# Performance work log

Measured on AMD Instinct MI355X. Metric: run time of the kernel, lower is better.

## Reference

```python
import jax, jax.numpy as jnp
import numpy as np

B, D, C, P = 64, 262144, 4, 4096  # batch, original_dim, c, proj_dim


def setup_inputs() -> dict:
    key = jax.random.key(0)
    kx, ki, ks = jax.random.split(key, 3)
    x = jax.random.normal(kx, (B, D), dtype=jnp.float32)
    rand_indices = jax.random.randint(ki, (D, C), 0, P, dtype=jnp.int64)
    rand_sign_bits = jax.random.randint(ks, (D, C), 0, 2, dtype=jnp.int32)
    return {"x": x, "rand_indices": rand_indices, "rand_sign_bits": rand_sign_bits}


def reference(x, rand_indices, rand_sign_bits):
    # signs in {-1, +1}, matching (randint(0,2)*2 - 1) in the torch module
    signs = (2 * rand_sign_bits - 1).astype(x.dtype)          # [D, C]
    idx = rand_indices.reshape(-1)                             # [D*C]
    vals = (x[:, :, None] * signs[None, :, :]).reshape(x.shape[0], -1)  # [B, D*C]
    # scatter-add each signed value into its hashed projection slot
    project = lambda v: jax.ops.segment_sum(v, idx, num_segments=P)
    return jax.vmap(project)(vals)                             # [B, P]
```

## Files before the change

### kernel.cpp

```cpp
#include <hip/hip_runtime.h>
#include <hip/hip_bf16.h>
#include <hip/hip_fp16.h>


constexpr int B_DIM = 64;
constexpr int D_DIM = 262144;
constexpr int P_DIM = 4096;

constexpr int NDS   = 64;
constexpr int SLICE = D_DIM / NDS;
constexpr int NBIN  = 16;
constexpr int NSC   = 16;
constexpr int SC_D  = SLICE / NSC;
constexpr int BCAP  = 128;
constexpr int NHB   = 32;
constexpr int WPB   = 8;
constexpr int PR_W  = 16;
constexpr int NPR   = P_DIM / PR_W;
constexpr int LCAP  = 128;

constexpr size_t REG_OFF   = 0;
constexpr size_t REG_BYTES = (size_t)NDS * NSC * NBIN * BCAP * 4;
constexpr size_t CNT_OFF   = REG_OFF + REG_BYTES;
constexpr size_t CNT_BYTES = (size_t)NDS * NSC * NBIN * 4;
constexpr size_t XT_OFF    = CNT_OFF + CNT_BYTES;
constexpr size_t XT_BYTES  = (size_t)D_DIM * B_DIM * 2;
constexpr size_t PART_OFF  = XT_OFF + XT_BYTES;
constexpr size_t PART_BYTES = (size_t)NPR * NDS * PR_W * B_DIM * 2;
constexpr size_t WS_NEED   = PART_OFF + PART_BYTES;

__global__ __launch_bounds__(512) void k_binpack(
    const int* __restrict__ idx, const int* __restrict__ sgn,
    unsigned* __restrict__ reg, int* __restrict__ cnt) {
    const int w = threadIdx.x >> 6, lane = threadIdx.x & 63;
    const int dslice = blockIdx.x >> 1;
    const int half   = blockIdx.x & 1;
    const int sc     = half * 8 + w;
    const int d0     = dslice * SLICE + sc * SC_D;
    unsigned* regw = reg + ((size_t)(dslice * NSC + sc) * NBIN) * BCAP;
    const unsigned long long lmask = (1ull << lane) - 1ull;

    unsigned cb[16];
    #pragma unroll
    for (int b = 0; b < 16; ++b) cb[b] = 0;

    #pragma unroll
    for (int step = 0; step < SC_D / 64; ++step) {
        const int dli = step * 64 + lane;
        const int4 iv = reinterpret_cast<const int4*>(idx)[d0 + dli];
        const int4 sv = reinterpret_cast<const int4*>(sgn)[d0 + dli];
        const unsigned rowbyte = (unsigned)((sc * SC_D + dli) << 7);
        #pragma unroll
        for (int c = 0; c < 4; ++c) {
            const unsigned p = ((unsigned)((c==0)?iv.x:(c==1)?iv.y:(c==2)?iv.z:iv.w)) & 4095u;
            const unsigned s = ((unsigned)((c==0)?sv.x:(c==1)?sv.y:(c==2)?sv.z:sv.w)) & 1u;
            const unsigned e = rowbyte | ((p & 255u) << 19) | ((s ^ 1u) << 31);
            const unsigned bin = p >> 8;
            unsigned pos = 0;
            #pragma unroll
            for (int b = 0; b < 16; ++b) {
                const unsigned long long m = __ballot(bin == (unsigned)b);
                if (bin == (unsigned)b) pos = cb[b] + (unsigned)__popcll(m & lmask);
                cb[b] += (unsigned)__popcll(m);
            }
            if (pos < (unsigned)BCAP) regw[bin * BCAP + pos] = e;
        }
    }
    unsigned cval = 0;
    #pragma unroll
    for (int b = 0; b < 16; ++b) {
        const unsigned cc = cb[b] < (unsigned)BCAP ? cb[b] : (unsigned)BCAP;
        cval = (lane == b) ? cc : cval;
    }
    if (lane < 16) cnt[(dslice * NSC + sc) * NBIN + lane] = (int)cval;
}

__device__ __forceinline__ unsigned short f32_to_bf16_rne(float f) {
    unsigned u = __float_as_uint(f);
    u += 0x7FFFu + ((u >> 16) & 1u);
    return (unsigned short)(u >> 16);
}

__global__ __launch_bounds__(256) void k_transpose(
    const float* __restrict__ x, unsigned short* __restrict__ xTb) {
    __shared__ float tile[64 * 65];
    const int d0 = blockIdx.x * 64;
    const int t = threadIdx.x;
    const int lane = t & 63;
    #pragma unroll
    for (int k = 0; k < 16; ++k) {
        const int b = k * 4 + (t >> 6);
        tile[lane * 65 + b] = x[(size_t)b * D_DIM + d0 + lane];
    }
    __syncthreads();
    #pragma unroll
    for (int k = 0; k < 16; ++k) {
        const int dr = k * 4 + (t >> 6);
        xTb[(size_t)(d0 + dr) * B_DIM + lane] = f32_to_bf16_rne(tile[dr * 65 + lane]);
    }
}

__global__ __launch_bounds__(512, 8) void k_process(
    const unsigned* __restrict__ reg, const int* __restrict__ cnt,
    const unsigned short* __restrict__ xTb, __half* __restrict__ part) {
    __shared__ __half2 hist[WPB][2 * PR_W * 32];
    __shared__ unsigned lst[WPB][LCAP];
    __shared__ int cnts[WPB][WPB];
    __shared__ int baseL[WPB][WPB];
    __shared__ int totals[WPB];

    const int w = threadIdx.x >> 6, lane = threadIdx.x & 63;
    const int dslice = blockIdx.x & 63;
    const int hb  = blockIdx.x >> 6;
    const int bin = hb >> 1, half = hb & 1;

    __half2* hw = hist[w];
    {
        unsigned* h32 = reinterpret_cast<unsigned*>(hw);
        #pragma unroll
        for (int k = 0; k < 16; ++k) h32[k * 64 + lane] = 0u;
    }

    const unsigned long long lmask = (1ull << lane) - 1ull;

    unsigned er[4];
    int n0 = 0, n1 = 0;
    int c0 = 0, c1 = 0, c2 = 0, c3 = 0, c4 = 0, c5 = 0, c6 = 0, c7 = 0;
    #pragma unroll
    for (int sc2 = 0; sc2 < 2; ++sc2) {
        const int sc = 2 * w + sc2;
        const int n  = cnt[(dslice * NSC + sc) * NBIN + bin];
        const unsigned* list = reg + ((size_t)((dslice * NSC + sc) * NBIN + bin)) * BCAP;
        if (sc2 == 0) n0 = n; else n1 = n;
        #pragma unroll
        for (int b = 0; b < 2; ++b) {
            const int i = b * 64 + lane;
            const unsigned e = (i < n) ? list[i] : 0u;
            er[sc2 * 2 + b] = e;
            const unsigned po8 = (e >> 19) & 255u;
            const bool valid = (i < n) && ((int)(po8 >> 7) == half);
            const unsigned t = valid ? ((po8 >> 4) & 7u) : 0xFFu;
            const unsigned long long m0 = __ballot(t == 0u);
            const unsigned long long m1 = __ballot(t == 1u);
            const unsigned long long m2 = __ballot(t == 2u);
            const unsigned long long m3 = __ballot(t == 3u);
            const unsigned long long m4 = __ballot(t == 4u);
            const unsigned long long m5 = __ballot(t == 5u);
            const unsigned long long m6 = __ballot(t == 6u);
            const unsigned long long m7 = __ballot(t == 7u);
            c0 += __popcll(m0); c1 += __popcll(m1);
            c2 += __popcll(m2); c3 += __popcll(m3);
            c4 += __popcll(m4); c5 += __popcll(m5);
            c6 += __popcll(m6); c7 += __popcll(m7);
        }
    }
    {
        int cval = 0;
        cval = (lane == 0) ? c0 : cval; cval = (lane == 1) ? c1 : cval;
        cval = (lane == 2) ? c2 : cval; cval = (lane == 3) ? c3 : cval;
        cval = (lane == 4) ? c4 : cval; cval = (lane == 5) ? c5 : cval;
        cval = (lane == 6) ? c6 : cval; cval = (lane == 7) ? c7 : cval;
        if (lane < 8) cnts[w][lane] = cval;
    }
    __syncthreads();

    if (w == 0 && lane < 8) {
        int run = 0;
        #pragma unroll
        for (int ww = 0; ww < 8; ++ww) { baseL[lane][ww] = run; run += cnts[ww][lane]; }
        totals[lane] = run;
    }
    __syncthreads();

    c0 = c1 = c2 = c3 = c4 = c5 = c6 = c7 = 0;
    #pragma unroll
    for (int sc2 = 0; sc2 < 2; ++sc2) {
        const int n = (sc2 == 0) ? n0 : n1;
        #pragma unroll
        for (int b = 0; b < 2; ++b) {
            const int i = b * 64 + lane;
            const unsigned e = er[sc2 * 2 + b];
            const unsigned po8 = (e >> 19) & 255u;
            const bool valid = (i < n) && ((int)(po8 >> 7) == half);
            const unsigned t = valid ? ((po8 >> 4) & 7u) : 0xFFu;
            const unsigned long long m0 = __ballot(t == 0u);
            const unsigned long long m1 = __ballot(t == 1u);
            const unsigned long long m2 = __ballot(t == 2u);
            const unsigned long long m3 = __ballot(t == 3u);
            const unsigned long long m4 = __ballot(t == 4u);
            const unsigned long long m5 = __ballot(t == 5u);
            const unsigned long long m6 = __ballot(t == 6u);
            const unsigned long long m7 = __ballot(t == 7u);
            if (valid) {
                const unsigned long long mt =
                    t < 4u ? (t < 2u ? (t == 0u ? m0 : m1) : (t == 2u ? m2 : m3))
                           : (t < 6u ? (t == 4u ? m4 : m5) : (t == 6u ? m6 : m7));
                const int cbase =
                    t < 4u ? (t < 2u ? (t == 0u ? c0 : c1) : (t == 2u ? c2 : c3))
                           : (t < 6u ? (t == 4u ? c4 : c5) : (t == 6u ? c6 : c7));
                const int pos = baseL[t][w] + cbase + (int)__popcll(mt & lmask);
                if (pos < LCAP) lst[t][pos] = e;
            }
            c0 += __popcll(m0); c1 += __popcll(m1);
            c2 += __popcll(m2); c3 += __popcll(m3);
            c4 += __popcll(m4); c5 += __popcll(m5);
            c6 += __popcll(m6); c7 += __popcll(m7);
        }
    }
    __syncthreads();

    const char* xs_c = reinterpret_cast<const char*>(xTb) + (size_t)dslice * SLICE * 128;
    const unsigned li4 = (unsigned)(lane & 31) * 4u;
    const bool hi = lane >= 32;
    const unsigned l31 = (unsigned)(lane & 31);
    const int n = totals[w] < LCAP ? totals[w] : LCAP;
    const unsigned* L = lst[w];

    int i = 0;
    for (; i + 8 <= n; i += 8) {
        const uint4 A  = *reinterpret_cast<const uint4*>(L + i);
        const uint4 Bv = *reinterpret_cast<const uint4*>(L + i + 4);
        const unsigned e0 = __builtin_amdgcn_readfirstlane(A.x);
        const unsigned e1 = __builtin_amdgcn_readfirstlane(A.y);
        const unsigned e2 = __builtin_amdgcn_readfirstlane(A.z);
        const unsigned e3 = __builtin_amdgcn_readfirstlane(A.w);
        const unsigned e4 = __builtin_amdgcn_readfirstlane(Bv.x);
        const unsigned e5 = __builtin_amdgcn_readfirstlane(Bv.y);
        const unsigned e6 = __builtin_amdgcn_readfirstlane(Bv.z);
        const unsigned e7 = __builtin_amdgcn_readfirstlane(Bv.w);
        const unsigned va0 = (hi ? (e4 & 0x7FFFFu) : (e0 & 0x7FFFFu)) + li4;
        const unsigned va1 = (hi ? (e5 & 0x7FFFFu) : (e1 & 0x7FFFFu)) + li4;
        const unsigned va2 = (hi ? (e6 & 0x7FFFFu) : (e2 & 0x7FFFFu)) + li4;
        const unsigned va3 = (hi ? (e7 & 0x7FFFFu) : (e3 & 0x7FFFFu)) + li4;
        const unsigned d0 = *reinterpret_cast<const unsigned*>(xs_c + va0);
        const unsigned d1 = *reinterpret_cast<const unsigned*>(xs_c + va1);
        const unsigned d2 = *reinterpret_cast<const unsigned*>(xs_c + va2);
        const unsigned d3 = *reinterpret_cast<const unsigned*>(xs_c + va3);

        const unsigned pL0 = (e0 >> 19) & 15u, pL1 = (e1 >> 19) & 15u;
        const unsigned pL2 = (e2 >> 19) & 15u, pL3 = (e3 >> 19) & 15u;
        const unsigned pH0 = (e4 >> 19) & 15u, pH1 = (e5 >> 19) & 15u;
        const unsigned pH2 = (e6 >> 19) & 15u, pH3 = (e7 >> 19) & 15u;

        __half2 v[4];
        #pragma unroll
        for (int k = 0; k < 4; ++k) {
            const unsigned dv = (k == 0) ? d0 : (k == 1) ? d1 : (k == 2) ? d2 : d3;
            const unsigned eL = (k == 0) ? e0 : (k == 1) ? e1 : (k == 2) ? e2 : e3;
            const unsigned eH = (k == 0) ? e4 : (k == 1) ? e5 : (k == 2) ? e6 : e7;
            const float flo = __uint_as_float(dv << 16);
            const float fhh = __uint_as_float(dv & 0xFFFF0000u);
            unsigned pkb = __builtin_bit_cast(unsigned, __floats2half2_rn(flo, fhh));
            const unsigned sm = hi ? (eH & 0x80000000u) : (eL & 0x80000000u);
            pkb ^= sm ? 0x80008000u : 0u;
            v[k] = __builtin_bit_cast(__half2, pkb);
        }

        const __half2 zero2 = __builtin_bit_cast(__half2, 0u);
        {
            const bool m01 = hi ? (pH0 == pH1) : (pL0 == pL1);
            v[1] = m01 ? __hadd2(v[1], v[0]) : v[1];  v[0] = m01 ? zero2 : v[0];
            const bool m02 = hi ? (pH0 == pH2) : (pL0 == pL2);
            v[2] = m02 ? __hadd2(v[2], v[0]) : v[2];  v[0] = m02 ? zero2 : v[0];
            const bool m12 = hi ? (pH1 == pH2) : (pL1 == pL2);
            v[2] = m12 ? __hadd2(v[2], v[1]) : v[2];  v[1] = m12 ? zero2 : v[1];
            const bool m03 = hi ? (pH0 == pH3) : (pL0 == pL3);
            v[3] = m03 ? __hadd2(v[3], v[0]) : v[3];  v[0] = m03 ? zero2 : v[0];
            const bool m13 = hi ? (pH1 == pH3) : (pL1 == pL3);
            v[3] = m13 ? __hadd2(v[3], v[1]) : v[3];  v[1] = m13 ? zero2 : v[1];
            const bool m23 = hi ? (pH2 == pH3) : (pL2 == pL3);
            v[3] = m23 ? __hadd2(v[3], v[2]) : v[3];  v[2] = m23 ? zero2 : v[2];
        }

        const unsigned a0 = (hi ? (512u + pH0 * 32u) : (pL0 * 32u)) + l31;
        const unsigned a1 = (hi ? (512u + pH1 * 32u) : (pL1 * 32u)) + l31;
        const unsigned a2 = (hi ? (512u + pH2 * 32u) : (pL2 * 32u)) + l31;
        const unsigned a3 = (hi ? (512u + pH3 * 32u) : (pL3 * 32u)) + l31;
        const __half2 h0 = hw[a0];
        const __half2 h1 = hw[a1];
        const __half2 h2v = hw[a2];
        const __half2 h3 = hw[a3];
        hw[a0] = __hadd2(h0, v[0]);
        hw[a1] = __hadd2(h1, v[1]);
        hw[a2] = __hadd2(h2v, v[2]);
        hw[a3] = __hadd2(h3, v[3]);
    }
    for (; i + 2 <= n; i += 2) {
        const unsigned eA = __builtin_amdgcn_readfirstlane(L[i]);
        const unsigned eB = __builtin_amdgcn_readfirstlane(L[i + 1]);
        const unsigned va = (hi ? (eB & 0x7FFFFu) : (eA & 0x7FFFFu)) + li4;
        const unsigned dv = *reinterpret_cast<const unsigned*>(xs_c + va);
        const float flo = __uint_as_float(dv << 16);
        const float fhh = __uint_as_float(dv & 0xFFFF0000u);
        unsigned pkb = __builtin_bit_cast(unsigned, __floats2half2_rn(flo, fhh));
        const unsigned sm = hi ? (eB & 0x80000000u) : (eA & 0x80000000u);
        pkb ^= sm ? 0x80008000u : 0u;
        const unsigned po = hi ? ((eB >> 19) & 15u) : ((eA >> 19) & 15u);
        const unsigned a = (hi ? (512u + po * 32u) : (po * 32u)) + l31;
        hw[a] = __hadd2(hw[a], __builtin_bit_cast(__half2, pkb));
    }
    if (i < n) {
        const unsigned eA = __builtin_amdgcn_readfirstlane(L[i]);
        if (!hi) {
            const unsigned va = (eA & 0x7FFFFu) + li4;
            const unsigned dv = *reinterpret_cast<const unsigned*>(xs_c + va);
            const float flo = __uint_as_float(dv << 16);
            const float fhh = __uint_as_float(dv & 0xFFFF0000u);
            unsigned pkb = __builtin_bit_cast(unsigned, __floats2half2_rn(flo, fhh));
            pkb ^= (eA & 0x80000000u) ? 0x80008000u : 0u;
            const unsigned a = ((eA >> 19) & 15u) * 32u + l31;
            hw[a] = __hadd2(hw[a], __builtin_bit_cast(__half2, pkb));
        }
    }

    unsigned* wp32 = reinterpret_cast<unsigned*>(
        part + ((size_t)((hb * WPB + w) * NDS + dslice)) * (PR_W * B_DIM));
    #pragma unroll
    for (int k = 0; k < 8; ++k) {
        const int idxw = k * 64 + lane;
        const __half2 s = __hadd2(hw[idxw], hw[512 + idxw]);
        wp32[idxw] = __builtin_bit_cast(unsigned, s);
    }
}

__global__ __launch_bounds__(256) void k_reduce(
    const __half* __restrict__ part, float* __restrict__ out) {
    const int pr = blockIdx.x;
    const int t  = threadIdx.x;

    float4 acc = make_float4(0.f, 0.f, 0.f, 0.f);
    const size_t base = (size_t)pr * NDS * (PR_W * B_DIM);
    for (int ds = 0; ds < NDS; ++ds) {
        const uint2 pv = *reinterpret_cast<const uint2*>(
            part + base + (size_t)ds * (PR_W * B_DIM) + t * 4);
        const __half2 h0 = __builtin_bit_cast(__half2, pv.x);
        const __half2 h1 = __builtin_bit_cast(__half2, pv.y);
        acc.x += __half2float(h0.x); acc.y += __half2float(h0.y);
        acc.z += __half2float(h1.x); acc.w += __half2float(h1.y);
    }

    __shared__ float st[16][65];
    const int po = (t * 4) >> 6;
    const int b0 = (t * 4) & 63;
    st[po][b0]     = acc.x; st[po][b0 + 1] = acc.y;
    st[po][b0 + 2] = acc.z; st[po][b0 + 3] = acc.w;
    __syncthreads();

    #pragma unroll
    for (int k = 0; k < 4; ++k) {
        const int flat = k * 256 + t;
        const int b = flat >> 4, poo = flat & 15;
        out[(size_t)b * P_DIM + pr * PR_W + poo] = st[poo][b];
    }
}

__device__ __forceinline__ float signed_val(float x, int s) {
    return __uint_as_float(__float_as_uint(x) ^ (((unsigned)(s ^ 1)) << 31));
}

__global__ __launch_bounds__(1024) void sjlt_hist_fb(
    const float* __restrict__ x, const int* __restrict__ idx,
    const int* __restrict__ sgn, float* __restrict__ out) {
    __shared__ float hist[2][P_DIM];
    for (int i = threadIdx.x; i < 2 * P_DIM; i += 1024) (&hist[0][0])[i] = 0.0f;
    __syncthreads();
    const int chunk = blockIdx.x, bg = blockIdx.y;
    const int d0 = chunk * (D_DIM / 16), b0 = bg * 2;
    const float* xr0 = x + (size_t)b0 * D_DIM + d0;
    const float* xr1 = xr0 + D_DIM;
    const int4* iv4 = reinterpret_cast<const int4*>(idx) + d0;
    const int4* sv4 = reinterpret_cast<const int4*>(sgn) + d0;
    for (int t = threadIdx.x; t < D_DIM / 16; t += 1024) {
        const int4 iv = iv4[t]; const int4 sv = sv4[t];
        const float x0 = xr0[t], x1 = xr1[t];
        unsafeAtomicAdd(&hist[0][iv.x], signed_val(x0, sv.x));
        unsafeAtomicAdd(&hist[0][iv.y], signed_val(x0, sv.y));
        unsafeAtomicAdd(&hist[0][iv.z], signed_val(x0, sv.z));
        unsafeAtomicAdd(&hist[0][iv.w], signed_val(x0, sv.w));
        unsafeAtomicAdd(&hist[1][iv.x], signed_val(x1, sv.x));
        unsafeAtomicAdd(&hist[1][iv.y], signed_val(x1, sv.y));
        unsafeAtomicAdd(&hist[1][iv.z], signed_val(x1, sv.z));
        unsafeAtomicAdd(&hist[1][iv.w], signed_val(x1, sv.w));
    }
    __syncthreads();
    float* o = out + (size_t)b0 * P_DIM;
    for (int p = threadIdx.x; p < P_DIM; p += 1024) {
        unsafeAtomicAdd(&o[p],         hist[0][p]);
        unsafeAtomicAdd(&o[P_DIM + p], hist[1][p]);
    }
}

extern "C" void kernel_launch(void* const* d_in, const int* in_sizes, int n_in,
                              void* d_out, int out_size, void* d_ws, size_t ws_size,
                              hipStream_t stream) {
    const float* x   = (const float*)d_in[0];
    const int*   idx = (const int*)d_in[1];
    const int*   sgn = (const int*)d_in[2];
    float* out = (float*)d_out;

    if (ws_size >= WS_NEED) {
        char* ws = (char*)d_ws;
        unsigned* reg = (unsigned*)(ws + REG_OFF);
        int* cnt      = (int*)(ws + CNT_OFF);
        unsigned short* xTb = (unsigned short*)(ws + XT_OFF);
        __half* part  = (__half*)(ws + PART_OFF);

        k_binpack<<<NDS * 2, 512, 0, stream>>>(idx, sgn, reg, cnt);
        k_transpose<<<D_DIM / 64, 256, 0, stream>>>(x, xTb);
        k_process<<<NHB * NDS, 512, 0, stream>>>(reg, cnt, xTb, part);
        k_reduce<<<NPR, 256, 0, stream>>>(part, out);
    } else {
        hipMemsetAsync(d_out, 0, (size_t)out_size * sizeof(float), stream);
        dim3 grid(16, 32);
        sjlt_hist_fb<<<grid, 1024, 0, stream>>>(x, idx, sgn, out);
    }
}
```

Before: 77.11 us.

## Group d-slices per process block, store x as fp16, split binpack finer

Each k_process block now loops over four d-slices and accumulates into its shared-memory histogram before writing partials. This cuts the partial buffer and the k_reduce work by a factor of four, at the cost of fewer, longer blocks and extra barriers inside the loop. The transpose now stores x as fp16 rather than bf16, so the per-element bf16-to-fp16 conversion in the inner loop becomes a plain sign XOR. This changes rounding and fp16 range behaviour. k_binpack is relaunched as 256-thread blocks with four blocks per slice, giving more and smaller blocks.

```diff
diff --git a/kernel.cpp b/kernel.cpp
--- a/kernel.cpp
+++ b/kernel.cpp
@@ -14,6 +14,8 @@
 constexpr int SC_D  = SLICE / NSC;
 constexpr int BCAP  = 128;
 constexpr int NHB   = 32;
+constexpr int G_DS  = 4;
+constexpr int NDG   = NDS / G_DS;
 constexpr int WPB   = 8;
 constexpr int PR_W  = 16;
 constexpr int NPR   = P_DIM / PR_W;
@@ -26,17 +28,17 @@
 constexpr size_t XT_OFF    = CNT_OFF + CNT_BYTES;
 constexpr size_t XT_BYTES  = (size_t)D_DIM * B_DIM * 2;
 constexpr size_t PART_OFF  = XT_OFF + XT_BYTES;
-constexpr size_t PART_BYTES = (size_t)NPR * NDS * PR_W * B_DIM * 2;
+constexpr size_t PART_BYTES = (size_t)NPR * NDG * PR_W * B_DIM * 2;
 constexpr size_t WS_NEED   = PART_OFF + PART_BYTES;
 
-__global__ __launch_bounds__(512) void k_binpack(
+__global__ __launch_bounds__(256) void k_binpack(
     const int* __restrict__ idx, const int* __restrict__ sgn,
     unsigned* __restrict__ reg, int* __restrict__ cnt) {
     const int w = threadIdx.x >> 6, lane = threadIdx.x & 63;
-    const int dslice = blockIdx.x >> 1;
-    const int half   = blockIdx.x & 1;
-    const int sc     = half * 8 + w;
-    const int d0     = dslice * SLICE + sc * SC_D;
+    const int dslice  = blockIdx.x >> 2;
+    const int quarter = blockIdx.x & 3;
+    const int sc      = quarter * 4 + w;
+    const int d0      = dslice * SLICE + sc * SC_D;
     unsigned* regw = reg + ((size_t)(dslice * NSC + sc) * NBIN) * BCAP;
     const unsigned long long lmask = (1ull << lane) - 1ull;
 
@@ -75,14 +77,8 @@
     if (lane < 16) cnt[(dslice * NSC + sc) * NBIN + lane] = (int)cval;
 }
 
-__device__ __forceinline__ unsigned short f32_to_bf16_rne(float f) {
-    unsigned u = __float_as_uint(f);
-    u += 0x7FFFu + ((u >> 16) & 1u);
-    return (unsigned short)(u >> 16);
-}
-
 __global__ __launch_bounds__(256) void k_transpose(
-    const float* __restrict__ x, unsigned short* __restrict__ xTb) {
+    const float* __restrict__ x, unsigned short* __restrict__ xTh) {
     __shared__ float tile[64 * 65];
     const int d0 = blockIdx.x * 64;
     const int t = threadIdx.x;
@@ -96,13 +92,14 @@
     #pragma unroll
     for (int k = 0; k < 16; ++k) {
         const int dr = k * 4 + (t >> 6);
-        xTb[(size_t)(d0 + dr) * B_DIM + lane] = f32_to_bf16_rne(tile[dr * 65 + lane]);
+        const __half h = __float2half_rn(tile[dr * 65 + lane]);
+        xTh[(size_t)(d0 + dr) * B_DIM + lane] = __builtin_bit_cast(unsigned short, h);
     }
 }
 
 __global__ __launch_bounds__(512, 8) void k_process(
     const unsigned* __restrict__ reg, const int* __restrict__ cnt,
-    const unsigned short* __restrict__ xTb, __half* __restrict__ part) {
+    const unsigned short* __restrict__ xTh, __half* __restrict__ part) {
     __shared__ __half2 hist[WPB][2 * PR_W * 32];
     __shared__ unsigned lst[WPB][LCAP];
     __shared__ int cnts[WPB][WPB];
@@ -110,8 +107,8 @@
     __shared__ int totals[WPB];
 
     const int w = threadIdx.x >> 6, lane = threadIdx.x & 63;
-    const int dslice = blockIdx.x & 63;
-    const int hb  = blockIdx.x >> 6;
+    const int dg  = blockIdx.x & 15;
+    const int hb  = blockIdx.x >> 4;
     const int bin = hb >> 1, half = hb & 1;
 
     __half2* hw = hist[w];
@@ -122,199 +119,187 @@
     }
 
     const unsigned long long lmask = (1ull << lane) - 1ull;
-
-    unsigned er[4];
-    int n0 = 0, n1 = 0;
-    int c0 = 0, c1 = 0, c2 = 0, c3 = 0, c4 = 0, c5 = 0, c6 = 0, c7 = 0;
-    #pragma unroll
-    for (int sc2 = 0; sc2 < 2; ++sc2) {
-        const int sc = 2 * w + sc2;
-        const int n  = cnt[(dslice * NSC + sc) * NBIN + bin];
-        const unsigned* list = reg + ((size_t)((dslice * NSC + sc) * NBIN + bin)) * BCAP;
-        if (sc2 == 0) n0 = n; else n1 = n;
-        #pragma unroll
-        for (int b = 0; b < 2; ++b) {
-            const int i = b * 64 + lane;
-            const unsigned e = (i < n) ? list[i] : 0u;
-            er[sc2 * 2 + b] = e;
-            const unsigned po8 = (e >> 19) & 255u;
-            const bool valid = (i < n) && ((int)(po8 >> 7) == half);
-            const unsigned t = valid ? ((po8 >> 4) & 7u) : 0xFFu;
-            const unsigned long long m0 = __ballot(t == 0u);
-            const unsigned long long m1 = __ballot(t == 1u);
-            const unsigned long long m2 = __ballot(t == 2u);
-            const unsigned long long m3 = __ballot(t == 3u);
-            const unsigned long long m4 = __ballot(t == 4u);
-            const unsigned long long m5 = __ballot(t == 5u);
-            const unsigned long long m6 = __ballot(t == 6u);
-            const unsigned long long m7 = __ballot(t == 7u);
-            c0 += __popcll(m0); c1 += __popcll(m1);
-            c2 += __popcll(m2); c3 += __popcll(m3);
-            c4 += __popcll(m4); c5 += __popcll(m5);
-            c6 += __popcll(m6); c7 += __popcll(m7);
-        }
-    }
-    {
-        int cval = 0;
-        cval = (lane == 0) ? c0 : cval; cval = (lane == 1) ? c1 : cval;
-        cval = (lane == 2) ? c2 : cval; cval = (lane == 3) ? c3 : cval;
-        cval = (lane == 4) ? c4 : cval; cval = (lane == 5) ? c5 : cval;
-        cval = (lane == 6) ? c6 : cval; cval = (lane == 7) ? c7 : cval;
-        if (lane < 8) cnts[w][lane] = cval;
-    }
-    __syncthreads();
-
-    if (w == 0 && lane < 8) {
-        int run = 0;
-        #pragma unroll
-        for (int ww = 0; ww < 8; ++ww) { baseL[lane][ww] = run; run += cnts[ww][lane]; }
-        totals[lane] = run;
-    }
-    __syncthreads();
-
-    c0 = c1 = c2 = c3 = c4 = c5 = c6 = c7 = 0;
-    #pragma unroll
-    for (int sc2 = 0; sc2 < 2; ++sc2) {
-        const int n = (sc2 == 0) ? n0 : n1;
-        #pragma unroll
-        for (int b = 0; b < 2; ++b) {
-            const int i = b * 64 + lane;
-            const unsigned e = er[sc2 * 2 + b];
-            const unsigned po8 = (e >> 19) & 255u;
-            const bool valid = (i < n) && ((int)(po8 >> 7) == half);
-            const unsigned t = valid ? ((po8 >> 4) & 7u) : 0xFFu;
-            const unsigned long long m0 = __ballot(t == 0u);
-            const unsigned long long m1 = __ballot(t == 1u);
-            const unsigned long long m2 = __ballot(t == 2u);
-            const unsigned long long m3 = __ballot(t == 3u);
-            const unsigned long long m4 = __ballot(t == 4u);
-            const unsigned long long m5 = __ballot(t == 5u);
-            const unsigned long long m6 = __ballot(t == 6u);
-            const unsigned long long m7 = __ballot(t == 7u);
-            if (valid) {
-                const unsigned long long mt =
-                    t < 4u ? (t < 2u ? (t == 0u ? m0 : m1) : (t == 2u ? m2 : m3))
-                           : (t < 6u ? (t == 4u ? m4 : m5) : (t == 6u ? m6 : m7));
-                const int cbase =
-                    t < 4u ? (t < 2u ? (t == 0u ? c0 : c1) : (t == 2u ? c2 : c3))
-                           : (t < 6u ? (t == 4u ? c4 : c5) : (t == 6u ? c6 : c7));
-                const int pos = baseL[t][w] + cbase + (int)__popcll(mt & lmask);
-                if (pos < LCAP) lst[t][pos] = e;
-            }
-            c0 += __popcll(m0); c1 += __popcll(m1);
-            c2 += __popcll(m2); c3 += __popcll(m3);
-            c4 += __popcll(m4); c5 += __popcll(m5);
-            c6 += __popcll(m6); c7 += __popcll(m7);
-        }
-    }
-    __syncthreads();
-
-    const char* xs_c = reinterpret_cast<const char*>(xTb) + (size_t)dslice * SLICE * 128;
     const unsigned li4 = (unsigned)(lane & 31) * 4u;
     const bool hi = lane >= 32;
     const unsigned l31 = (unsigned)(lane & 31);
-    const int n = totals[w] < LCAP ? totals[w] : LCAP;
-    const unsigned* L = lst[w];
-
-    int i = 0;
-    for (; i + 8 <= n; i += 8) {
-        const uint4 A  = *reinterpret_cast<const uint4*>(L + i);
-        const uint4 Bv = *reinterpret_cast<const uint4*>(L + i + 4);
-        const unsigned e0 = __builtin_amdgcn_readfirstlane(A.x);
-        const unsigned e1 = __builtin_amdgcn_readfirstlane(A.y);
-        const unsigned e2 = __builtin_amdgcn_readfirstlane(A.z);
-        const unsigned e3 = __builtin_amdgcn_readfirstlane(A.w);
-        const unsigned e4 = __builtin_amdgcn_readfirstlane(Bv.x);
-        const unsigned e5 = __builtin_amdgcn_readfirstlane(Bv.y);
-        const unsigned e6 = __builtin_amdgcn_readfirstlane(Bv.z);
-        const unsigned e7 = __builtin_amdgcn_readfirstlane(Bv.w);
-        const unsigned va0 = (hi ? (e4 & 0x7FFFFu) : (e0 & 0x7FFFFu)) + li4;
-        const unsigned va1 = (hi ? (e5 & 0x7FFFFu) : (e1 & 0x7FFFFu)) + li4;
-        const unsigned va2 = (hi ? (e6 & 0x7FFFFu) : (e2 & 0x7FFFFu)) + li4;
-        const unsigned va3 = (hi ? (e7 & 0x7FFFFu) : (e3 & 0x7FFFFu)) + li4;
-        const unsigned d0 = *reinterpret_cast<const unsigned*>(xs_c + va0);
-        const unsigned d1 = *reinterpret_cast<const unsigned*>(xs_c + va1);
-        const unsigned d2 = *reinterpret_cast<const unsigned*>(xs_c + va2);
-        const unsigned d3 = *reinterpret_cast<const unsigned*>(xs_c + va3);
-
-        const unsigned pL0 = (e0 >> 19) & 15u, pL1 = (e1 >> 19) & 15u;
-        const unsigned pL2 = (e2 >> 19) & 15u, pL3 = (e3 >> 19) & 15u;
-        const unsigned pH0 = (e4 >> 19) & 15u, pH1 = (e5 >> 19) & 15u;
-        const unsigned pH2 = (e6 >> 19) & 15u, pH3 = (e7 >> 19) & 15u;
-
-        __half2 v[4];
+
+    for (int ds = 0; ds < G_DS; ++ds) {
+        const int dslice = dg * G_DS + ds;
+
+        unsigned er[4];
+        int n0 = 0, n1 = 0;
+        int c0 = 0, c1 = 0, c2 = 0, c3 = 0, c4 = 0, c5 = 0, c6 = 0, c7 = 0;
         #pragma unroll
-        for (int k = 0; k < 4; ++k) {
-            const unsigned dv = (k == 0) ? d0 : (k == 1) ? d1 : (k == 2) ? d2 : d3;
-            const unsigned eL = (k == 0) ? e0 : (k == 1) ? e1 : (k == 2) ? e2 : e3;
-            const unsigned eH = (k == 0) ? e4 : (k == 1) ? e5 : (k == 2) ? e6 : e7;
-            const float flo = __uint_as_float(dv << 16);
-            const float fhh = __uint_as_float(dv & 0xFFFF0000u);
-            unsigned pkb = __builtin_bit_cast(unsigned, __floats2half2_rn(flo, fhh));
-            const unsigned sm = hi ? (eH & 0x80000000u) : (eL & 0x80000000u);
-            pkb ^= sm ? 0x80008000u : 0u;
-            v[k] = __builtin_bit_cast(__half2, pkb);
-        }
-
-        const __half2 zero2 = __builtin_bit_cast(__half2, 0u);
+        for (int sc2 = 0; sc2 < 2; ++sc2) {
+            const int sc = 2 * w + sc2;
+            const int n  = cnt[(dslice * NSC + sc) * NBIN + bin];
+            const unsigned* list = reg + ((size_t)((dslice * NSC + sc) * NBIN + bin)) * BCAP;
+            if (sc2 == 0) n0 = n; else n1 = n;
+            #pragma unroll
+            for (int b = 0; b < 2; ++b) {
+                const int i = b * 64 + lane;
+                const unsigned e = (i < n) ? list[i] : 0u;
+                er[sc2 * 2 + b] = e;
+                const unsigned po8 = (e >> 19) & 255u;
+                const bool valid = (i < n) && ((int)(po8 >> 7) == half);
+                const unsigned t = valid ? ((po8 >> 4) & 7u) : 0xFFu;
+                c0 += __popcll(__ballot(t == 0u)); c1 += __popcll(__ballot(t == 1u));
+                c2 += __popcll(__ballot(t == 2u)); c3 += __popcll(__ballot(t == 3u));
+                c4 += __popcll(__ballot(t == 4u)); c5 += __popcll(__ballot(t == 5u));
+                c6 += __popcll(__ballot(t == 6u)); c7 += __popcll(__ballot(t == 7u));
+            }
+        }
         {
-            const bool m01 = hi ? (pH0 == pH1) : (pL0 == pL1);
-            v[1] = m01 ? __hadd2(v[1], v[0]) : v[1];  v[0] = m01 ? zero2 : v[0];
-            const bool m02 = hi ? (pH0 == pH2) : (pL0 == pL2);
-            v[2] = m02 ? __hadd2(v[2], v[0]) : v[2];  v[0] = m02 ? zero2 : v[0];
-            const bool m12 = hi ? (pH1 == pH2) : (pL1 == pL2);
-            v[2] = m12 ? __hadd2(v[2], v[1]) : v[2];  v[1] = m12 ? zero2 : v[1];
-            const bool m03 = hi ? (pH0 == pH3) : (pL0 == pL3);
-            v[3] = m03 ? __hadd2(v[3], v[0]) : v[3];  v[0] = m03 ? zero2 : v[0];
-            const bool m13 = hi ? (pH1 == pH3) : (pL1 == pL3);
-            v[3] = m13 ? __hadd2(v[3], v[1]) : v[3];  v[1] = m13 ? zero2 : v[1];
-            const bool m23 = hi ? (pH2 == pH3) : (pL2 == pL3);
-            v[3] = m23 ? __hadd2(v[3], v[2]) : v[3];  v[2] = m23 ? zero2 : v[2];
-        }
-
-        const unsigned a0 = (hi ? (512u + pH0 * 32u) : (pL0 * 32u)) + l31;
-        const unsigned a1 = (hi ? (512u + pH1 * 32u) : (pL1 * 32u)) + l31;
-        const unsigned a2 = (hi ? (512u + pH2 * 32u) : (pL2 * 32u)) + l31;
-        const unsigned a3 = (hi ? (512u + pH3 * 32u) : (pL3 * 32u)) + l31;
-        const __half2 h0 = hw[a0];
-        const __half2 h1 = hw[a1];
-        const __half2 h2v = hw[a2];
-        const __half2 h3 = hw[a3];
-        hw[a0] = __hadd2(h0, v[0]);
-        hw[a1] = __hadd2(h1, v[1]);
-        hw[a2] = __hadd2(h2v, v[2]);
-        hw[a3] = __hadd2(h3, v[3]);
-    }
-    for (; i + 2 <= n; i += 2) {
-        const unsigned eA = __builtin_amdgcn_readfirstlane(L[i]);
-        const unsigned eB = __builtin_amdgcn_readfirstlane(L[i + 1]);
-        const unsigned va = (hi ? (eB & 0x7FFFFu) : (eA & 0x7FFFFu)) + li4;
-        const unsigned dv = *reinterpret_cast<const unsigned*>(xs_c + va);
-        const float flo = __uint_as_float(dv << 16);
-        const float fhh = __uint_as_float(dv & 0xFFFF0000u);
-        unsigned pkb = __builtin_bit_cast(unsigned, __floats2half2_rn(flo, fhh));
-        const unsigned sm = hi ? (eB & 0x80000000u) : (eA & 0x80000000u);
-        pkb ^= sm ? 0x80008000u : 0u;
-        const unsigned po = hi ? ((eB >> 19) & 15u) : ((eA >> 19) & 15u);
-        const unsigned a = (hi ? (512u + po * 32u) : (po * 32u)) + l31;
-        hw[a] = __hadd2(hw[a], __builtin_bit_cast(__half2, pkb));
-    }
-    if (i < n) {
-        const unsigned eA = __builtin_amdgcn_readfirstlane(L[i]);
-        if (!hi) {
-            const unsigned va = (eA & 0x7FFFFu) + li4;
+            int cval = 0;
+            cval = (lane == 0) ? c0 : cval; cval = (lane == 1) ? c1 : cval;
+            cval = (lane == 2) ? c2 : cval; cval = (lane == 3) ? c3 : cval;
+            cval = (lane == 4) ? c4 : cval; cval = (lane == 5) ? c5 : cval;
+            cval = (lane == 6) ? c6 : cval; cval = (lane == 7) ? c7 : cval;
+            if (lane < 8) cnts[w][lane] = cval;
+        }
+        __syncthreads();
+
+        if (w == 0 && lane < 8) {
+            int run = 0;
+            #pragma unroll
+            for (int ww = 0; ww < 8; ++ww) { baseL[lane][ww] = run; run += cnts[ww][lane]; }
+            totals[lane] = run;
+        }
+        __syncthreads();
+
+        c0 = c1 = c2 = c3 = c4 = c5 = c6 = c7 = 0;
+        #pragma unroll
+        for (int sc2 = 0; sc2 < 2; ++sc2) {
+            const int n = (sc2 == 0) ? n0 : n1;
+            #pragma unroll
+            for (int b = 0; b < 2; ++b) {
+                const int i = b * 64 + lane;
+                const unsigned e = er[sc2 * 2 + b];
+                const unsigned po8 = (e >> 19) & 255u;
+                const bool valid = (i < n) && ((int)(po8 >> 7) == half);
+                const unsigned t = valid ? ((po8 >> 4) & 7u) : 0xFFu;
+                const unsigned long long m0 = __ballot(t == 0u);
+                const unsigned long long m1 = __ballot(t == 1u);
+                const unsigned long long m2 = __ballot(t == 2u);
+                const unsigned long long m3 = __ballot(t == 3u);
+                const unsigned long long m4 = __ballot(t == 4u);
+                const unsigned long long m5 = __ballot(t == 5u);
+                const unsigned long long m6 = __ballot(t == 6u);
+                const unsigned long long m7 = __ballot(t == 7u);
+                if (valid) {
+                    const unsigned long long mt =
+                        t < 4u ? (t < 2u ? (t == 0u ? m0 : m1) : (t == 2u ? m2 : m3))
+                               : (t < 6u ? (t == 4u ? m4 : m5) : (t == 6u ? m6 : m7));
+                    const int cbase =
+                        t < 4u ? (t < 2u ? (t == 0u ? c0 : c1) : (t == 2u ? c2 : c3))
+                               : (t < 6u ? (t == 4u ? c4 : c5) : (t == 6u ? c6 : c7));
+                    const int pos = baseL[t][w] + cbase + (int)__popcll(mt & lmask);
+                    if (pos < LCAP) lst[t][pos] = e;
+                }
+                c0 += __popcll(m0); c1 += __popcll(m1);
+                c2 += __popcll(m2); c3 += __popcll(m3);
+                c4 += __popcll(m4); c5 += __popcll(m5);
+                c6 += __popcll(m6); c7 += __popcll(m7);
+            }
+        }
+        __syncthreads();
+
+        const char* xs_c = reinterpret_cast<const char*>(xTh) + (size_t)dslice * SLICE * 128;
+        const int n = totals[w] < LCAP ? totals[w] : LCAP;
+        const unsigned* L = lst[w];
+
+        int i = 0;
+        for (; i + 8 <= n; i += 8) {
+            const uint4 A  = *reinterpret_cast<const uint4*>(L + i);
+            const uint4 Bv = *reinterpret_cast<const uint4*>(L + i + 4);
+            const unsigned e0 = __builtin_amdgcn_readfirstlane(A.x);
+            const unsigned e1 = __builtin_amdgcn_readfirstlane(A.y);
+            const unsigned e2 = __builtin_amdgcn_readfirstlane(A.z);
+            const unsigned e3 = __builtin_amdgcn_readfirstlane(A.w);
+            const unsigned e4 = __builtin_amdgcn_readfirstlane(Bv.x);
+            const unsigned e5 = __builtin_amdgcn_readfirstlane(Bv.y);
+            const unsigned e6 = __builtin_amdgcn_readfirstlane(Bv.z);
+            const unsigned e7 = __builtin_amdgcn_readfirstlane(Bv.w);
+            const unsigned va0 = (hi ? (e4 & 0x7FFFFu) : (e0 & 0x7FFFFu)) + li4;
+            const unsigned va1 = (hi ? (e5 & 0x7FFFFu) : (e1 & 0x7FFFFu)) + li4;
+            const unsigned va2 = (hi ? (e6 & 0x7FFFFu) : (e2 & 0x7FFFFu)) + li4;
+            const unsigned va3 = (hi ? (e7 & 0x7FFFFu) : (e3 & 0x7FFFFu)) + li4;
+            const unsigned d0 = *reinterpret_cast<const unsigned*>(xs_c + va0);
+            const unsigned d1 = *reinterpret_cast<const unsigned*>(xs_c + va1);
+            const unsigned d2 = *reinterpret_cast<const unsigned*>(xs_c + va2);
+            const unsigned d3 = *reinterpret_cast<const unsigned*>(xs_c + va3);
+
+            const unsigned pL0 = (e0 >> 19) & 15u, pL1 = (e1 >> 19) & 15u;
+            const unsigned pL2 = (e2 >> 19) & 15u, pL3 = (e3 >> 19) & 15u;
+            const unsigned pH0 = (e4 >> 19) & 15u, pH1 = (e5 >> 19) & 15u;
+            const unsigned pH2 = (e6 >> 19) & 15u, pH3 = (e7 >> 19) & 15u;
+
+            __half2 v[4];
+            #pragma unroll
+            for (int k = 0; k < 4; ++k) {
+                const unsigned dv = (k == 0) ? d0 : (k == 1) ? d1 : (k == 2) ? d2 : d3;
+                const unsigned eL = (k == 0) ? e0 : (k == 1) ? e1 : (k == 2) ? e2 : e3;
+                const unsigned eH = (k == 0) ? e4 : (k == 1) ? e5 : (k == 2) ? e6 : e7;
+                const unsigned sm = hi ? (eH & 0x80000000u) : (eL & 0x80000000u);
+                v[k] = __builtin_bit_cast(__half2, dv ^ (sm ? 0x80008000u : 0u));
+            }
+
+            const __half2 zero2 = __builtin_bit_cast(__half2, 0u);
+            {
+                const bool m01 = hi ? (pH0 == pH1) : (pL0 == pL1);
+                v[1] = m01 ? __hadd2(v[1], v[0]) : v[1];  v[0] = m01 ? zero2 : v[0];
+                const bool m02 = hi ? (pH0 == pH2) : (pL0 == pL2);
+                v[2] = m02 ? __hadd2(v[2], v[0]) : v[2];  v[0] = m02 ? zero2 : v[0];
+                const bool m12 = hi ? (pH1 == pH2) : (pL1 == pL2);
+                v[2] = m12 ? __hadd2(v[2], v[1]) : v[2];  v[1] = m12 ? zero2 : v[1];
+                const bool m03 = hi ? (pH0 == pH3) : (pL0 == pL3);
+                v[3] = m03 ? __hadd2(v[3], v[0]) : v[3];  v[0] = m03 ? zero2 : v[0];
+                const bool m13 = hi ? (pH1 == pH3) : (pL1 == pL3);
+                v[3] = m13 ? __hadd2(v[3], v[1]) : v[3];  v[1] = m13 ? zero2 : v[1];
+                const bool m23 = hi ? (pH2 == pH3) : (pL2 == pL3);
+                v[3] = m23 ? __hadd2(v[3], v[2]) : v[3];  v[2] = m23 ? zero2 : v[2];
+            }
+
+            const unsigned a0 = (hi ? (512u + pH0 * 32u) : (pL0 * 32u)) + l31;
+            const unsigned a1 = (hi ? (512u + pH1 * 32u) : (pL1 * 32u)) + l31;
+            const unsigned a2 = (hi ? (512u + pH2 * 32u) : (pL2 * 32u)) + l31;
+            const unsigned a3 = (hi ? (512u + pH3 * 32u) : (pL3 * 32u)) + l31;
+            const __half2 h0 = hw[a0];
+            const __half2 h1 = hw[a1];
+            const __half2 h2v = hw[a2];
+            const __half2 h3 = hw[a3];
+            hw[a0] = __hadd2(h0, v[0]);
+            hw[a1] = __hadd2(h1, v[1]);
+            hw[a2] = __hadd2(h2v, v[2]);
+            hw[a3] = __hadd2(h3, v[3]);
+        }
+        for (; i + 2 <= n; i += 2) {
+            const unsigned eA = __builtin_amdgcn_readfirstlane(L[i]);
+            const unsigned eB = __builtin_amdgcn_readfirstlane(L[i + 1]);
+            const unsigned va = (hi ? (eB & 0x7FFFFu) : (eA & 0x7FFFFu)) + li4;
             const unsigned dv = *reinterpret_cast<const unsigned*>(xs_c + va);
-            const float flo = __uint_as_float(dv << 16);
-            const float fhh = __uint_as_float(dv & 0xFFFF0000u);
-            unsigned pkb = __builtin_bit_cast(unsigned, __floats2half2_rn(flo, fhh));
-            pkb ^= (eA & 0x80000000u) ? 0x80008000u : 0u;
-            const unsigned a = ((eA >> 19) & 15u) * 32u + l31;
-            hw[a] = __hadd2(hw[a], __builtin_bit_cast(__half2, pkb));
-        }
+            const unsigned sm = hi ? (eB & 0x80000000u) : (eA & 0x80000000u);
+            const __half2 v2 = __builtin_bit_cast(__half2, dv ^ (sm ? 0x80008000u : 0u));
+            const unsigned po = hi ? ((eB >> 19) & 15u) : ((eA >> 19) & 15u);
+            const unsigned a = (hi ? (512u + po * 32u) : (po * 32u)) + l31;
+            hw[a] = __hadd2(hw[a], v2);
+        }
+        if (i < n) {
+            const unsigned eA = __builtin_amdgcn_readfirstlane(L[i]);
+            if (!hi) {
+                const unsigned va = (eA & 0x7FFFFu) + li4;
+                const unsigned dv = *reinterpret_cast<const unsigned*>(xs_c + va);
+                const __half2 v2 = __builtin_bit_cast(__half2,
+                    dv ^ ((eA & 0x80000000u) ? 0x80008000u : 0u));
+                const unsigned a = ((eA >> 19) & 15u) * 32u + l31;
+                hw[a] = __hadd2(hw[a], v2);
+            }
+        }
+        __syncthreads();
     }
 
     unsigned* wp32 = reinterpret_cast<unsigned*>(
-        part + ((size_t)((hb * WPB + w) * NDS + dslice)) * (PR_W * B_DIM));
+        part + ((size_t)((hb * WPB + w) * NDG + dg)) * (PR_W * B_DIM));
     #pragma unroll
     for (int k = 0; k < 8; ++k) {
         const int idxw = k * 64 + lane;
@@ -329,10 +314,10 @@
     const int t  = threadIdx.x;
 
     float4 acc = make_float4(0.f, 0.f, 0.f, 0.f);
-    const size_t base = (size_t)pr * NDS * (PR_W * B_DIM);
-    for (int ds = 0; ds < NDS; ++ds) {
+    const size_t base = (size_t)pr * NDG * (PR_W * B_DIM);
+    for (int dgi = 0; dgi < NDG; ++dgi) {
         const uint2 pv = *reinterpret_cast<const uint2*>(
-            part + base + (size_t)ds * (PR_W * B_DIM) + t * 4);
+            part + base + (size_t)dgi * (PR_W * B_DIM) + t * 4);
         const __half2 h0 = __builtin_bit_cast(__half2, pv.x);
         const __half2 h1 = __builtin_bit_cast(__half2, pv.y);
         acc.x += __half2float(h0.x); acc.y += __half2float(h0.y);
@@ -402,12 +387,12 @@
         char* ws = (char*)d_ws;
         unsigned* reg = (unsigned*)(ws + REG_OFF);
         int* cnt      = (int*)(ws + CNT_OFF);
-        unsigned short* xTb = (unsigned short*)(ws + XT_OFF);
+        unsigned short* xTh = (unsigned short*)(ws + XT_OFF);
         __half* part  = (__half*)(ws + PART_OFF);
 
-        k_binpack<<<NDS * 2, 512, 0, stream>>>(idx, sgn, reg, cnt);
-        k_transpose<<<D_DIM / 64, 256, 0, stream>>>(x, xTb);
-        k_process<<<NHB * NDS, 512, 0, stream>>>(reg, cnt, xTb, part);
+        k_binpack<<<NDS * 4, 256, 0, stream>>>(idx, sgn, reg, cnt);
+        k_transpose<<<D_DIM / 64, 256, 0, stream>>>(x, xTh);
+        k_process<<<NHB * NDG, 512, 0, stream>>>(reg, cnt, xTh, part);
         k_reduce<<<NPR, 256, 0, stream>>>(part, out);
     } else {
         hipMemsetAsync(d_out, 0, (size_t)out_size * sizeof(float), stream);
```

Result: no change. 78.50 us (+1.8%).
